# Kernel optimization log

Hardware: AMD Instinct MI355X
Metric: run time of the kernel (lower is better)

The kernel has to match this reference:

```python
import jax, jax.numpy as jnp
import numpy as np

B, N, D, E = 2, 512, 128, 64
H, HS, FF = 8, 16, 512
EPS = 1e-6

def _glorot(key, shape, fan_in, fan_out):
    limit = np.sqrt(6.0 / (fan_in + fan_out))
    return jax.random.uniform(key, shape, jnp.float32, -limit, limit)

def setup_inputs() -> dict:
    key = jax.random.key(0)
    ks = jax.random.split(key, 12)
    node = jax.random.normal(ks[0], (B, N, D), jnp.float32)
    edge = jax.random.normal(ks[1], (B, N, N, E), jnp.float32)
    Wq = _glorot(ks[2], (H, D, HS), D, HS)
    Wk = _glorot(ks[3], (H, D + E, HS), D + E, HS)
    Wv = _glorot(ks[4], (H, D, HS), D, HS)
    Wp = _glorot(ks[5], (H, HS, D), H * HS, D)
    bp = jnp.zeros((D,), jnp.float32)
    ln1_g = jnp.ones((D,), jnp.float32)
    ln1_b = jnp.zeros((D,), jnp.float32)
    Wf1 = _glorot(ks[6], (D, FF), D, FF)
    bf1 = jnp.zeros((FF,), jnp.float32)
    Wf2 = _glorot(ks[7], (FF, D), FF, D)
    bf2 = jnp.zeros((D,), jnp.float32)
    ln2_g = jnp.ones((D,), jnp.float32)
    ln2_b = jnp.zeros((D,), jnp.float32)
    return dict(node=node, edge=edge, Wq=Wq, Wk=Wk, Wv=Wv, Wp=Wp, bp=bp,
                ln1_g=ln1_g, ln1_b=ln1_b, Wf1=Wf1, bf1=bf1, Wf2=Wf2, bf2=bf2,
                ln2_g=ln2_g, ln2_b=ln2_b)

def _layernorm(x, g, b):
    mu = jnp.mean(x, axis=-1, keepdims=True)
    var = jnp.mean(jnp.square(x - mu), axis=-1, keepdims=True)
    return (x - mu) * jax.lax.rsqrt(var + EPS) * g + b

def reference(node, edge, Wq, Wk, Wv, Wp, bp, ln1_g, ln1_b, Wf1, bf1, Wf2, bf2, ln2_g, ln2_b):
    # --- edge-conditioned multi-head attention ---
    # query scaled by sqrt(head_size), as in the TF code
    q = jnp.einsum('bni,hio->bnho', node, Wq) / jnp.sqrt(jnp.asarray(HS, node.dtype))
    # concat([repeat(key), edge]) @ Wk  ==  key @ Wk[:, :D]  +  edge @ Wk[:, D:]
    Wk_node, Wk_edge = Wk[:, :D, :], Wk[:, D:, :]
    k_node = jnp.einsum('bmi,hio->bmho', node, Wk_node)           # [B,M,H,HS]
    logits_node = jnp.einsum('bnho,bmho->bhnm', q, k_node)        # [B,H,N,M]
    # contract q with edge-kernel first (small), then with edge (memory-bound pass)
    qe = jnp.einsum('bnho,heo->bnhe', q, Wk_edge)                 # [B,N,H,E]
    logits_edge = jnp.einsum('bnme,bnhe->bhnm', edge, qe)         # [B,H,N,M]
    attn = jax.nn.softmax(logits_node + logits_edge, axis=-1)
    v = jnp.einsum('bmi,hio->bmho', node, Wv)                     # [B,M,H,HS]
    mh = jnp.einsum('bhnm,bmho->bnho', attn, v)                   # [B,N,H,HS]
    attn_out = jnp.einsum('bnho,hoi->bni', mh, Wp) + bp           # [B,N,D]
    # --- residual + layernorm ---
    x = _layernorm(node + attn_out, ln1_g, ln1_b)
    # --- FFN: relu dense -> dense, residual + layernorm ---
    ff = jnp.maximum(x @ Wf1 + bf1, 0.0) @ Wf2 + bf2
    return _layernorm(x + ff, ln2_g, ln2_b)
```

## Files before the change

kernel.cpp:

```cpp
#include <hip/hip_runtime.h>
#include <cstdint>
#include <cmath>

#define BB 2
#define NN 512
#define DD 128
#define EE 64
#define HH 8
#define HSS 16
#define FFF 512
#define EPSF 1e-6f

__global__ __launch_bounds__(256)
void qkv_kernel(const float* __restrict__ node,
                const float* __restrict__ Wq,
                const float* __restrict__ Wk,
                const float* __restrict__ Wv,
                float* __restrict__ q_g,
                float* __restrict__ k_t,
                float* __restrict__ v_t,
                float* __restrict__ qe_g) {
  int r0 = blockIdx.x * 2;
  int t = threadIdx.x;
  int b = r0 >> 9;
  int n0 = r0 & 511;
  __shared__ float nrow[2][DD];
  __shared__ float qrow[2][DD];

  nrow[t >> 7][t & 127] = node[(size_t)r0*DD + t];
  __syncthreads();

  if (t < 128) {
    int h = t >> 4, o = t & 15;
    float aq[2] = {0.f,0.f}, av[2] = {0.f,0.f};
    const float* wq = Wq + h*(DD*HSS) + o;
    const float* wv = Wv + h*(DD*HSS) + o;
    for (int i = 0; i < DD; ++i) {
      float wqi = wq[i*HSS], wvi = wv[i*HSS];
      #pragma unroll
      for (int r = 0; r < 2; ++r) {
        float x = nrow[r][i];
        aq[r] += x * wqi;
        av[r] += x * wvi;
      }
    }
    #pragma unroll
    for (int r = 0; r < 2; ++r) {
      float qq = aq[r] * 0.25f;
      q_g[(size_t)(r0+r)*128 + t] = qq;
      qrow[r][t] = qq;
    }
    *(float2*)(v_t + ((size_t)(b*HH + (t>>4))*HSS + (t&15))*NN + n0) =
        make_float2(av[0], av[1]);
  } else {
    int tt = t - 128, h = tt >> 4, o = tt & 15;
    float ak[2] = {0.f,0.f};
    const float* wk = Wk + h*((DD+EE)*HSS) + o;
    for (int i = 0; i < DD; ++i) {
      float wki = wk[i*HSS];
      #pragma unroll
      for (int r = 0; r < 2; ++r) ak[r] += nrow[r][i] * wki;
    }
    *(float2*)(k_t + ((size_t)(b*HH + h)*HSS + o)*NN + n0) = make_float2(ak[0], ak[1]);
  }
  __syncthreads();

  for (int idx = t; idx < HH*EE; idx += 256) {
    int h = idx >> 6, e = idx & 63;
    const float* wke = Wk + (h*(DD+EE) + DD + e)*HSS;
    float w[HSS];
    #pragma unroll
    for (int o = 0; o < 16; ++o) w[o] = wke[o];
    #pragma unroll
    for (int r = 0; r < 2; ++r) {
      float a = 0.f;
      #pragma unroll
      for (int o = 0; o < 16; ++o) a += qrow[r][h*HSS + o] * w[o];
      qe_g[(size_t)(r0+r)*(HH*EE) + idx] = a;
    }
  }
}

__global__ __launch_bounds__(512)
void attn_kernel(const float* __restrict__ node,
                 const float* __restrict__ edge,
                 const float* __restrict__ q_g,
                 const float* __restrict__ k_t,
                 const float* __restrict__ v_t,
                 const float* __restrict__ qe_g,
                 const float* __restrict__ Wp,
                 const float* __restrict__ bp,
                 const float* __restrict__ ln1_g,
                 const float* __restrict__ ln1_b,
                 float* __restrict__ x_g) {
  int bn = blockIdx.x;
  int b = bn >> 9;
  int t = threadIdx.x;
  int h = t >> 6, ml = t & 63;
  __shared__ float4 et[2][64][16];
  __shared__ float mh_s[HH*HSS];
  __shared__ float red[4];

  float4 qe_r[16];
  const float4* qep = (const float4*)(qe_g + (size_t)bn*(HH*EE) + h*EE);
  #pragma unroll
  for (int j = 0; j < 16; ++j) qe_r[j] = qep[j];
  float q_r[16];
  const float* qp = q_g + (size_t)bn*128 + h*HSS;
  #pragma unroll
  for (int o = 0; o < 16; ++o) q_r[o] = qp[o];

  const float4* e_base = (const float4*)(edge + (size_t)bn*NN*EE);
  const float* kt_base = k_t + (size_t)(b*HH + h)*HSS*NN;
  const float* vt_base = v_t + (size_t)(b*HH + h)*HSS*NN;

  int ra = t >> 4,          ja = t & 15;   int ca = (ja + ra) & 15;
  int rb = (t + 512) >> 4,  jb = t & 15;   int cb = (jb + rb) & 15;

  float4 f0 = e_base[(size_t)ra*16 + ja];
  float4 f1 = e_base[(size_t)rb*16 + jb];

  float lg[8];
  for (int c = 0; c < 8; ++c) {
    int buf = c & 1;
    et[buf][ra][ca] = f0;
    et[buf][rb][cb] = f1;
    __syncthreads();
    if (c < 7) {
      f0 = e_base[(size_t)((c+1)*64 + ra)*16 + ja];
      f1 = e_base[(size_t)((c+1)*64 + rb)*16 + jb];
    }
    int m = c*64 + ml;
    float acc = 0.f;
    #pragma unroll
    for (int j = 0; j < 16; ++j) {
      float4 e4 = et[buf][ml][(j + ml) & 15];
      acc += e4.x*qe_r[j].x + e4.y*qe_r[j].y + e4.z*qe_r[j].z + e4.w*qe_r[j].w;
    }
    const float* kp = kt_base + m;
    #pragma unroll
    for (int o = 0; o < 16; ++o) acc += q_r[o] * kp[o*NN];
    lg[c] = acc;
  }

  float mx = lg[0];
  #pragma unroll
  for (int c = 1; c < 8; ++c) mx = fmaxf(mx, lg[c]);
  #pragma unroll
  for (int off = 1; off < 64; off <<= 1) mx = fmaxf(mx, __shfl_xor(mx, off, 64));
  float sum = 0.f;
  #pragma unroll
  for (int c = 0; c < 8; ++c) { lg[c] = __expf(lg[c] - mx); sum += lg[c]; }
  #pragma unroll
  for (int off = 1; off < 64; off <<= 1) sum += __shfl_xor(sum, off, 64);
  float inv = 1.f / sum;

  float mh_acc[16];
  #pragma unroll
  for (int z = 0; z < 16; ++z) mh_acc[z] = 0.f;
  for (int c = 0; c < 8; ++c) {
    float p = lg[c] * inv;
    const float* vp = vt_base + c*64 + ml;
    #pragma unroll
    for (int o = 0; o < 16; ++o) mh_acc[o] += p * vp[o*NN];
  }
  #pragma unroll
  for (int z = 0; z < 16; ++z) {
    #pragma unroll
    for (int off = 1; off < 64; off <<= 1)
      mh_acc[z] += __shfl_xor(mh_acc[z], off, 64);
  }
  if (ml == 0) {
    #pragma unroll
    for (int z = 0; z < 16; ++z) mh_s[h*16 + z] = mh_acc[z];
  }
  __syncthreads();

  float val = 0.f;
  if (t < 128) {
    float a = bp[t];
    #pragma unroll 4
    for (int ho = 0; ho < 128; ++ho) a += mh_s[ho] * Wp[ho*128 + t];
    val = node[(size_t)bn*128 + t] + a;
    float s1 = val, s2 = val*val;
    #pragma unroll
    for (int off = 1; off < 64; off <<= 1) {
      s1 += __shfl_xor(s1, off, 64);
      s2 += __shfl_xor(s2, off, 64);
    }
    if ((t & 63) == 0) { red[(t>>6)*2] = s1; red[(t>>6)*2 + 1] = s2; }
  }
  __syncthreads();
  if (t < 128) {
    float s1 = red[0] + red[2], s2 = red[1] + red[3];
    float mu = s1 * (1.f/128.f);
    float var = s2 * (1.f/128.f) - mu*mu;
    float xh = (val - mu) * rsqrtf(var + EPSF);
    x_g[(size_t)bn*128 + t] = xh * ln1_g[t] + ln1_b[t];
  }
}

__global__ __launch_bounds__(256)
void ffn_kernel(const float* __restrict__ x_g,
                const float* __restrict__ Wf1,
                const float* __restrict__ bf1,
                const float* __restrict__ Wf2,
                const float* __restrict__ bf2,
                const float* __restrict__ ln2_g,
                const float* __restrict__ ln2_b,
                float* __restrict__ out) {
  int t = threadIdx.x;
  int row0 = blockIdx.x * 2;
  __shared__ float xs[2][128];
  __shared__ float hs[2][FFF];
  __shared__ float ps[2][2][128];
  __shared__ float red2[4][2];

  ((float*)xs)[t] = x_g[(size_t)row0*128 + t];
  __syncthreads();

  float a00 = bf1[t], a01 = bf1[t + 256];
  float a10 = a00, a11 = a01;
  for (int i = 0; i < 128; ++i) {
    float w0 = Wf1[i*512 + t];
    float w1 = Wf1[i*512 + t + 256];
    float x0 = xs[0][i], x1 = xs[1][i];
    a00 += x0 * w0; a01 += x0 * w1;
    a10 += x1 * w0; a11 += x1 * w1;
  }
  hs[0][t]       = fmaxf(a00, 0.f);
  hs[0][t + 256] = fmaxf(a01, 0.f);
  hs[1][t]       = fmaxf(a10, 0.f);
  hs[1][t + 256] = fmaxf(a11, 0.f);
  __syncthreads();

  int i = t & 127, half = t >> 7;
  float p0 = 0.f, p1 = 0.f;
  for (int j = half*256; j < half*256 + 256; ++j) {
    float w = Wf2[j*128 + i];
    p0 += hs[0][j] * w;
    p1 += hs[1][j] * w;
  }
  ps[half][0][i] = p0;
  ps[half][1][i] = p1;
  __syncthreads();

  int rg = half;
  float va = bf2[i] + ps[0][rg][i] + ps[1][rg][i] + xs[rg][i];

  int w_ = t >> 6;
  float s1 = va, s2 = va*va;
  #pragma unroll
  for (int off = 1; off < 64; off <<= 1) {
    s1 += __shfl_xor(s1, off, 64);
    s2 += __shfl_xor(s2, off, 64);
  }
  if ((t & 63) == 0) { red2[w_][0] = s1; red2[w_][1] = s2; }
  __syncthreads();
  int pw = w_ ^ 1;
  float S1 = red2[w_][0] + red2[pw][0];
  float S2 = red2[w_][1] + red2[pw][1];
  float mu = S1 * (1.f/128.f);
  float var = S2 * (1.f/128.f) - mu*mu;
  out[((size_t)row0 + rg)*128 + i] =
      (va - mu) * rsqrtf(var + EPSF) * ln2_g[i] + ln2_b[i];
}

extern "C" void kernel_launch(void* const* d_in, const int* in_sizes, int n_in,
                              void* d_out, int out_size, void* d_ws, size_t ws_size,
                              hipStream_t stream) {
  const float* node  = (const float*)d_in[0];
  const float* edge  = (const float*)d_in[1];
  const float* Wq    = (const float*)d_in[2];
  const float* Wk    = (const float*)d_in[3];
  const float* Wv    = (const float*)d_in[4];
  const float* Wp    = (const float*)d_in[5];
  const float* bp    = (const float*)d_in[6];
  const float* ln1_g = (const float*)d_in[7];
  const float* ln1_b = (const float*)d_in[8];
  const float* Wf1   = (const float*)d_in[9];
  const float* bf1   = (const float*)d_in[10];
  const float* Wf2   = (const float*)d_in[11];
  const float* bf2   = (const float*)d_in[12];
  const float* ln2_g = (const float*)d_in[13];
  const float* ln2_b = (const float*)d_in[14];
  float* out = (float*)d_out;

  float* ws   = (float*)d_ws;
  float* q_g  = ws;
  float* qe_g = ws + 131072;
  float* k_t  = ws + 655360;
  float* v_t  = ws + 786432;
  float* x_g  = ws + 917504;

  qkv_kernel<<<(BB*NN)/2, 256, 0, stream>>>(node, Wq, Wk, Wv, q_g, k_t, v_t, qe_g);
  attn_kernel<<<BB*NN, 512, 0, stream>>>(node, edge, q_g, k_t, v_t, qe_g,
                                         Wp, bp, ln1_g, ln1_b, x_g);
  ffn_kernel<<<(BB*NN)/2, 256, 0, stream>>>(x_g, Wf1, bf1, Wf2, bf2,
                                            ln2_g, ln2_b, out);
}
```

Measured before the change: 325.4 us.

## Make per-head attention operands wave-uniform and raise occupancy bounds across kernels

The attention kernel now passes per-head q and qe values through readfirstlane, so the compiler can keep them in scalar registers instead of 80 vector registers per thread. The k-logit loop is hoisted out of the edge-tile loop, and the V accumulation is split into two halves of 8 outputs to cut live registers. All kernels also get launch_bounds minimum-occupancy hints and extra unroll pragmas. The aim is higher occupancy for the memory-bound edge pass; the risk is spills or a longer, serialized instruction stream.

After: 307.5 us. 1.06x faster.

```diff
diff --git a/kernel.cpp b/kernel.cpp
--- a/kernel.cpp
+++ b/kernel.cpp
@@ -11,7 +11,11 @@
 #define FFF 512
 #define EPSF 1e-6f
 
-__global__ __launch_bounds__(256)
+static __device__ __forceinline__ float rfl(float x) {
+  return __uint_as_float(__builtin_amdgcn_readfirstlane(__float_as_uint(x)));
+}
+
+__global__ __launch_bounds__(256, 8)
 void qkv_kernel(const float* __restrict__ node,
                 const float* __restrict__ Wq,
                 const float* __restrict__ Wk,
@@ -35,6 +39,7 @@
     float aq[2] = {0.f,0.f}, av[2] = {0.f,0.f};
     const float* wq = Wq + h*(DD*HSS) + o;
     const float* wv = Wv + h*(DD*HSS) + o;
+    #pragma unroll 8
     for (int i = 0; i < DD; ++i) {
       float wqi = wq[i*HSS], wvi = wv[i*HSS];
       #pragma unroll
@@ -56,6 +61,7 @@
     int tt = t - 128, h = tt >> 4, o = tt & 15;
     float ak[2] = {0.f,0.f};
     const float* wk = Wk + h*((DD+EE)*HSS) + o;
+    #pragma unroll 8
     for (int i = 0; i < DD; ++i) {
       float wki = wk[i*HSS];
       #pragma unroll
@@ -81,8 +87,10 @@
   }
 }
 
-__global__ __launch_bounds__(512)
-void attn_kernel(const float* __restrict__ node,
+template<bool HOIST>
+__global__ __launch_bounds__(512, 8)
+void attn_kernel(int bn_base,
+                 const float* __restrict__ node,
                  const float* __restrict__ edge,
                  const float* __restrict__ q_g,
                  const float* __restrict__ k_t,
@@ -93,7 +101,7 @@
                  const float* __restrict__ ln1_g,
                  const float* __restrict__ ln1_b,
                  float* __restrict__ x_g) {
-  int bn = blockIdx.x;
+  int bn = bn_base + blockIdx.x;
   int b = bn >> 9;
   int t = threadIdx.x;
   int h = t >> 6, ml = t & 63;
@@ -101,26 +109,48 @@
   __shared__ float mh_s[HH*HSS];
   __shared__ float red[4];
 
-  float4 qe_r[16];
-  const float4* qep = (const float4*)(qe_g + (size_t)bn*(HH*EE) + h*EE);
-  #pragma unroll
-  for (int j = 0; j < 16; ++j) qe_r[j] = qep[j];
-  float q_r[16];
-  const float* qp = q_g + (size_t)bn*128 + h*HSS;
-  #pragma unroll
-  for (int o = 0; o < 16; ++o) q_r[o] = qp[o];
+  float qe_s[64];
+  {
+    const float4* qep = (const float4*)(qe_g + (size_t)bn*(HH*EE) + h*EE);
+    #pragma unroll
+    for (int j = 0; j < 16; ++j) {
+      float4 v4 = qep[j];
+      if constexpr (HOIST) {
+        qe_s[4*j+0] = rfl(v4.x); qe_s[4*j+1] = rfl(v4.y);
+        qe_s[4*j+2] = rfl(v4.z); qe_s[4*j+3] = rfl(v4.w);
+      } else {
+        qe_s[4*j+0] = v4.x; qe_s[4*j+1] = v4.y;
+        qe_s[4*j+2] = v4.z; qe_s[4*j+3] = v4.w;
+      }
+    }
+  }
+  float q_s[16];
+  {
+    const float* qp = q_g + (size_t)bn*128 + h*HSS;
+    #pragma unroll
+    for (int o = 0; o < 16; ++o) q_s[o] = HOIST ? rfl(qp[o]) : qp[o];
+  }
 
   const float4* e_base = (const float4*)(edge + (size_t)bn*NN*EE);
   const float* kt_base = k_t + (size_t)(b*HH + h)*HSS*NN;
   const float* vt_base = v_t + (size_t)(b*HH + h)*HSS*NN;
 
-  int ra = t >> 4,          ja = t & 15;   int ca = (ja + ra) & 15;
-  int rb = (t + 512) >> 4,  jb = t & 15;   int cb = (jb + rb) & 15;
+  int ra = t >> 4,         ja = t & 15;   int ca = (ja + ra) & 15;
+  int rb = (t + 512) >> 4;                int cb = (ja + rb) & 15;
 
   float4 f0 = e_base[(size_t)ra*16 + ja];
-  float4 f1 = e_base[(size_t)rb*16 + jb];
+  float4 f1 = e_base[(size_t)rb*16 + ja];
 
   float lg[8];
+  #pragma unroll 2
+  for (int c = 0; c < 8; ++c) {
+    const float* kp = kt_base + c*64 + ml;
+    float a = 0.f;
+    #pragma unroll
+    for (int o = 0; o < 16; ++o) a += q_s[o] * kp[o*NN];
+    lg[c] = a;
+  }
+
   for (int c = 0; c < 8; ++c) {
     int buf = c & 1;
     et[buf][ra][ca] = f0;
@@ -128,19 +158,15 @@
     __syncthreads();
     if (c < 7) {
       f0 = e_base[(size_t)((c+1)*64 + ra)*16 + ja];
-      f1 = e_base[(size_t)((c+1)*64 + rb)*16 + jb];
-    }
-    int m = c*64 + ml;
+      f1 = e_base[(size_t)((c+1)*64 + rb)*16 + ja];
+    }
     float acc = 0.f;
     #pragma unroll
     for (int j = 0; j < 16; ++j) {
       float4 e4 = et[buf][ml][(j + ml) & 15];
-      acc += e4.x*qe_r[j].x + e4.y*qe_r[j].y + e4.z*qe_r[j].z + e4.w*qe_r[j].w;
-    }
-    const float* kp = kt_base + m;
-    #pragma unroll
-    for (int o = 0; o < 16; ++o) acc += q_r[o] * kp[o*NN];
-    lg[c] = acc;
+      acc += e4.x*qe_s[4*j+0] + e4.y*qe_s[4*j+1] + e4.z*qe_s[4*j+2] + e4.w*qe_s[4*j+3];
+    }
+    lg[c] += acc;
   }
 
   float mx = lg[0];
@@ -155,31 +181,34 @@
   for (int off = 1; off < 64; off <<= 1) sum += __shfl_xor(sum, off, 64);
   float inv = 1.f / sum;
 
-  float mh_acc[16];
-  #pragma unroll
-  for (int z = 0; z < 16; ++z) mh_acc[z] = 0.f;
-  for (int c = 0; c < 8; ++c) {
-    float p = lg[c] * inv;
-    const float* vp = vt_base + c*64 + ml;
-    #pragma unroll
-    for (int o = 0; o < 16; ++o) mh_acc[o] += p * vp[o*NN];
-  }
-  #pragma unroll
-  for (int z = 0; z < 16; ++z) {
-    #pragma unroll
-    for (int off = 1; off < 64; off <<= 1)
-      mh_acc[z] += __shfl_xor(mh_acc[z], off, 64);
-  }
-  if (ml == 0) {
-    #pragma unroll
-    for (int z = 0; z < 16; ++z) mh_s[h*16 + z] = mh_acc[z];
+  #pragma unroll
+  for (int half = 0; half < 2; ++half) {
+    float mh_acc[8];
+    #pragma unroll
+    for (int z = 0; z < 8; ++z) mh_acc[z] = 0.f;
+    for (int c = 0; c < 8; ++c) {
+      float p = lg[c] * inv;
+      const float* vp = vt_base + (size_t)half*8*NN + c*64 + ml;
+      #pragma unroll
+      for (int o = 0; o < 8; ++o) mh_acc[o] += p * vp[o*NN];
+    }
+    #pragma unroll
+    for (int z = 0; z < 8; ++z) {
+      #pragma unroll
+      for (int off = 1; off < 64; off <<= 1)
+        mh_acc[z] += __shfl_xor(mh_acc[z], off, 64);
+    }
+    if (ml == 0) {
+      #pragma unroll
+      for (int z = 0; z < 8; ++z) mh_s[h*16 + half*8 + z] = mh_acc[z];
+    }
   }
   __syncthreads();
 
   float val = 0.f;
   if (t < 128) {
     float a = bp[t];
-    #pragma unroll 4
+    #pragma unroll 8
     for (int ho = 0; ho < 128; ++ho) a += mh_s[ho] * Wp[ho*128 + t];
     val = node[(size_t)bn*128 + t] + a;
     float s1 = val, s2 = val*val;
@@ -200,7 +229,7 @@
   }
 }
 
-__global__ __launch_bounds__(256)
+__global__ __launch_bounds__(256, 8)
 void ffn_kernel(const float* __restrict__ x_g,
                 const float* __restrict__ Wf1,
                 const float* __restrict__ bf1,
@@ -221,6 +250,7 @@
 
   float a00 = bf1[t], a01 = bf1[t + 256];
   float a10 = a00, a11 = a01;
+  #pragma unroll 8
   for (int i = 0; i < 128; ++i) {
     float w0 = Wf1[i*512 + t];
     float w1 = Wf1[i*512 + t + 256];
@@ -236,6 +266,7 @@
 
   int i = t & 127, half = t >> 7;
   float p0 = 0.f, p1 = 0.f;
+  #pragma unroll 8
   for (int j = half*256; j < half*256 + 256; ++j) {
     float w = Wf2[j*128 + i];
     p0 += hs[0][j] * w;
@@ -294,8 +325,8 @@
   float* x_g  = ws + 917504;
 
   qkv_kernel<<<(BB*NN)/2, 256, 0, stream>>>(node, Wq, Wk, Wv, q_g, k_t, v_t, qe_g);
-  attn_kernel<<<BB*NN, 512, 0, stream>>>(node, edge, q_g, k_t, v_t, qe_g,
-                                         Wp, bp, ln1_g, ln1_b, x_g);
+  attn_kernel<true><<<BB*NN, 512, 0, stream>>>(0, node, edge, q_g, k_t, v_t, qe_g,
+                                               Wp, bp, ln1_g, ln1_b, x_g);
   ffn_kernel<<<(BB*NN)/2, 256, 0, stream>>>(x_g, Wf1, bf1, Wf2, bf2,
                                             ln2_g, ln2_b, out);
 }
```
